# Kernel tuning notes

Measured on AMD Instinct MI355X. Metric: run time of the kernel, lower is better.

Reference implementation:

```python
import jax, jax.numpy as jnp
import numpy as np

B, T, C, H, D = 2, 2048, 1024, 16, 64


def setup_inputs() -> dict:
    key = jax.random.key(0)
    k1, k2, k3, k4, k5 = jax.random.split(key, 5)
    x = jax.random.normal(k1, (B, T, C), dtype=jnp.float32)
    Wq = jax.random.normal(k2, (H, C, D), dtype=jnp.float32) * 0.02
    Wk = jax.random.normal(k3, (H, C, D), dtype=jnp.float32) * 0.02
    Wv = jax.random.normal(k4, (H, C, D), dtype=jnp.float32) * 0.02
    Wo = jax.random.normal(k5, (C, C), dtype=jnp.float32) * 0.02
    bo = jnp.zeros((C,), dtype=jnp.float32)
    return {"x": x, "Wq": Wq, "Wk": Wk, "Wv": Wv, "Wo": Wo, "bo": bo}


def reference(x, Wq, Wk, Wv, Wo, bo):
    # per-head projections (batched over heads instead of a python loop)
    q = jnp.einsum('btc,hcd->bhtd', x, Wq)
    k = jnp.einsum('btc,hcd->bhtd', x, Wk)
    v = jnp.einsum('btc,hcd->bhtd', x, Wv)
    scale = jnp.asarray(D, x.dtype) ** -0.5
    wei = jnp.einsum('bhtd,bhsd->bhts', q, k) * scale  # [B,H,T,T]
    causal = jnp.tril(jnp.ones((T, T), dtype=bool))
    wei = jnp.where(causal, wei, jnp.asarray(-jnp.inf, wei.dtype))
    attn = jax.nn.softmax(wei, axis=-1)
    out = jnp.einsum('bhts,bhsd->bhtd', attn, v)  # [B,H,T,D]
    # concat heads (head order h0..hH-1 along feature dim)
    out = out.transpose(0, 2, 1, 3).reshape(B, T, C)
    # output projection: nn.Linear -> y = x @ W^T + b  (dropout p=0 is identity)
    return out @ Wo.T + bo
```

## Files before the change

kernel.cpp:

```cpp
#include <hip/hip_runtime.h>
#include <hip/hip_bf16.h>
#include <cstdint>
#include <math.h>

#define B_DIM 2
#define T_SEQ 2048
#define C_DIM 1024
#define H_NUM 16
#define D_HEAD 64
#define M_ROWS (B_DIM * T_SEQ)
#define N_QKV (3 * H_NUM * D_HEAD)

using short8  = __attribute__((ext_vector_type(8))) short;
using short4v = __attribute__((ext_vector_type(4))) short;
using f32x4   = __attribute__((ext_vector_type(4))) float;

__device__ __forceinline__ short f2bf(float f) {
  union { __hip_bfloat16 h; short s; } u;
  u.h = __float2bfloat16(f);
  return u.s;
}

__device__ __forceinline__ unsigned pk2bf(float a, float b) {
  union { float f; unsigned u; } ua, ub;
  ua.f = a; ub.f = b;
  return __builtin_amdgcn_perm(ub.u, ua.u, 0x07060302u);
}

__device__ __forceinline__ void gld_lds16(short* lds, const short* g) {
  __builtin_amdgcn_global_load_lds(
      (const unsigned int __attribute__((address_space(1)))*)g,
      (unsigned int __attribute__((address_space(3)))*)lds, 16, 0, 0);
}

#define BAR_VM(N)                                                    \
  do {                                                               \
    asm volatile("s_waitcnt vmcnt(" #N ") lgkmcnt(0)" ::: "memory"); \
    __builtin_amdgcn_s_barrier();                                    \
    __builtin_amdgcn_sched_barrier(0);                               \
  } while (0)

__global__ __launch_bounds__(256) void cvt_f32_bf16(const float* __restrict__ in,
                                                    short* __restrict__ out, int n8) {
  int i = blockIdx.x * 256 + threadIdx.x;
  if (i >= n8) return;
  const float4* p = reinterpret_cast<const float4*>(in) + (size_t)i * 2;
  float4 a = p[0], b = p[1];
  short8 o;
  o[0] = f2bf(a.x); o[1] = f2bf(a.y); o[2] = f2bf(a.z); o[3] = f2bf(a.w);
  o[4] = f2bf(b.x); o[5] = f2bf(b.y); o[6] = f2bf(b.z); o[7] = f2bf(b.w);
  reinterpret_cast<short8*>(out)[i] = o;
}

__global__ __launch_bounds__(256) void pack_w(const float* __restrict__ Wq,
                                              const float* __restrict__ Wk,
                                              const float* __restrict__ Wv,
                                              short* __restrict__ Wt) {
  int bid  = blockIdx.x;
  int proj = bid >> 8;
  int h    = (bid >> 4) & 15;
  int cb   = bid & 15;
  const float* W = (proj == 0) ? Wq : ((proj == 1) ? Wk : Wv);
  const float* src = W + ((size_t)h * C_DIM + (size_t)cb * 64) * D_HEAD;

  __shared__ float tile[64][65];
  int tid = threadIdx.x;

#pragma unroll
  for (int j = 0; j < 4; j++) {
    int flat = tid + j * 256;
    int c    = flat >> 4;
    int d4   = flat & 15;
    float4 v = reinterpret_cast<const float4*>(src + (size_t)c * D_HEAD)[d4];
    tile[c][d4 * 4 + 0] = v.x;
    tile[c][d4 * 4 + 1] = v.y;
    tile[c][d4 * 4 + 2] = v.z;
    tile[c][d4 * 4 + 3] = v.w;
  }
  __syncthreads();

  int d     = tid >> 2;
  int cpart = (tid & 3) * 16;
  short* dst = Wt + ((size_t)(proj * H_NUM + h) * D_HEAD + d) * C_DIM + cb * 64 + cpart;
  short8 o0, o1;
#pragma unroll
  for (int j = 0; j < 8; j++) {
    o0[j] = f2bf(tile[cpart + j][d]);
    o1[j] = f2bf(tile[cpart + 8 + j][d]);
  }
  *reinterpret_cast<short8*>(dst)     = o0;
  *reinterpret_cast<short8*>(dst + 8) = o1;
}

template <int MODE, int BMT>
__global__ __launch_bounds__(256) void gemm_bt(
    const short* __restrict__ A, const short* __restrict__ Bt,
    const float* __restrict__ bias,
    short* __restrict__ qb, short* __restrict__ kb, short* __restrict__ vtb,
    float* __restrict__ outb,
    int M, int N, int K) {
  constexpr int BK = 32;
  constexpr int MR = BMT / 32;
  constexpr int NLA = BMT / 64;
  __shared__ short As[3][BMT * BK];
  __shared__ short Bs[3][128 * BK];

  int tid  = threadIdx.x;
  int lane = tid & 63;
  int wv   = tid >> 6;
  int q15  = lane & 15, g = lane >> 4;
  int ntn  = N >> 7;
  int bm   = blockIdx.x / ntn;
  int bn   = blockIdx.x % ntn;
  int row0 = bm * BMT, col0 = bn << 7;
  int wm   = (wv >> 1) * (BMT / 2);
  int wn   = (wv & 1) << 6;

  f32x4 acc[MR][4];
#pragma unroll
  for (int i = 0; i < MR; i++)
#pragma unroll
    for (int j = 0; j < 4; j++) acc[i][j] = (f32x4){0.f, 0.f, 0.f, 0.f};

  const short* ag = A  + (size_t)(row0 + (tid >> 2)) * K + (tid & 3) * 8;
  const short* bg = Bt + (size_t)(col0 + (tid >> 2)) * K + (tid & 3) * 8;
  const size_t gstep = (size_t)64 * K;

  auto stage = [&](int ks, int buf) {
    const short* a  = ag + (size_t)ks * BK;
    const short* bb = bg + (size_t)ks * BK;
    gld_lds16(&As[buf][0] + tid * 8, a);
    if constexpr (NLA == 2) gld_lds16(&As[buf][64 * BK] + tid * 8, a + gstep);
    gld_lds16(&Bs[buf][0] + tid * 8, bb);
    gld_lds16(&Bs[buf][64 * BK] + tid * 8, bb + gstep);
  };

  int nk = K / BK;
  stage(0, 0);
  stage(1, 1);
  if constexpr (NLA == 2) {
    asm volatile("s_waitcnt vmcnt(4)" ::: "memory");
  } else {
    asm volatile("s_waitcnt vmcnt(3)" ::: "memory");
  }
  __builtin_amdgcn_s_barrier();
  __builtin_amdgcn_sched_barrier(0);

  for (int k = 0; k < nk; ++k) {
    int buf = k % 3;
    if (k + 2 < nk) stage(k + 2, (k + 2) % 3);

    short8 af[MR], bf[4];
#pragma unroll
    for (int mi = 0; mi < MR; mi++)
      af[mi] = *reinterpret_cast<const short8*>(
          &As[buf][(wm + mi * 16 + q15) * BK + g * 8]);
#pragma unroll
    for (int ni = 0; ni < 4; ni++)
      bf[ni] = *reinterpret_cast<const short8*>(
          &Bs[buf][(wn + ni * 16 + q15) * BK + g * 8]);
    __builtin_amdgcn_s_setprio(1);
#pragma unroll
    for (int mi = 0; mi < MR; mi++)
#pragma unroll
      for (int ni = 0; ni < 4; ni++)
        acc[mi][ni] = __builtin_amdgcn_mfma_f32_16x16x32_bf16(af[mi], bf[ni],
                                                              acc[mi][ni], 0, 0, 0);
    __builtin_amdgcn_s_setprio(0);

    if (k + 1 < nk) {
      if (k + 2 < nk) {
        if constexpr (NLA == 2) { BAR_VM(4); } else { BAR_VM(3); }
      } else {
        BAR_VM(0);
      }
    }
  }

#pragma unroll
  for (int mi = 0; mi < MR; mi++) {
#pragma unroll
    for (int ni = 0; ni < 4; ni++) {
      int rb  = row0 + wm + mi * 16 + (g << 2);
      int col = col0 + wn + ni * 16 + q15;
      f32x4 v = acc[mi][ni];
      if (MODE == 0) {
        int proj = col >> 10;
        int hh   = (col >> 6) & (H_NUM - 1);
        int d    = col & (D_HEAD - 1);
        int b    = rb >> 11;
        int t    = rb & (T_SEQ - 1);
        if (proj < 2) {
          float scl = (proj == 0) ? 0.125f * 1.44269504f : 1.0f;
          short* dst = (proj == 0 ? qb : kb) +
                       ((size_t)(b * H_NUM + hh) * T_SEQ) * D_HEAD + d;
#pragma unroll
          for (int r = 0; r < 4; r++)
            dst[(size_t)(t + r) * D_HEAD] = f2bf(v[r] * scl);
        } else {
          short4v pk;
#pragma unroll
          for (int r = 0; r < 4; r++) pk[r] = f2bf(v[r]);
          short* dst = vtb + ((size_t)(b * H_NUM + hh) * D_HEAD + d) * T_SEQ + t;
          *reinterpret_cast<short4v*>(dst) = pk;
        }
      } else {
        float bb = bias[col];
#pragma unroll
        for (int r = 0; r < 4; r++)
          outb[(size_t)(rb + r) * N + col] = v[r] + bb;
      }
    }
  }
}

__global__ __launch_bounds__(256, 4) void attn_fwd(const short* __restrict__ qg,
                                                   const short* __restrict__ kg,
                                                   const short* __restrict__ vt,
                                                   short* __restrict__ ob) {
  int bid  = blockIdx.x;
  int q2   = bid >> 8;
  int r    = bid & 255;
  int bh   = (r & 7) * 4 + q2;
  int sb   = r >> 3;
  int strip = (q2 & 1) ? sb : 31 - sb;
  int b    = bh >> 4;
  int h    = bh & 15;
  int tid  = threadIdx.x, lane = tid & 63, wv = tid >> 6;
  int q15  = lane & 15, g = lane >> 4;
  int qr   = strip * 64 + wv * 16;

  __shared__ short arena[16384];

  const short* qp = qg + (size_t)bh * T_SEQ * D_HEAD;
  const short* kp = kg + (size_t)bh * T_SEQ * D_HEAD;
  const short* vp = vt + (size_t)bh * D_HEAD * T_SEQ;

  int r8    = lane >> 3;
  int gcb   = ((lane & 7) * 16) ^ (r8 << 4);
  int srow0 = wv * 16;

  int hh = (q15 & 7) << 4;
  int koff0 = ((0 * 64 + g * 16) ^ hh) >> 1;
  int koff1 = ((1 * 64 + g * 16) ^ hh) >> 1;
  int voff[4];
#pragma unroll
  for (int st = 0; st < 4; st++) voff[st] = ((st * 32 + g * 8) ^ hh) >> 1;

  short8 qf[2];
#pragma unroll
  for (int kk = 0; kk < 2; kk++)
    qf[kk] = *reinterpret_cast<const short8*>(
        qp + (size_t)(qr + q15) * D_HEAD + kk * 32 + g * 8);

  f32x4 acc[4];
#pragma unroll
  for (int dt = 0; dt < 4; dt++) acc[dt] = (f32x4){0.f, 0.f, 0.f, 0.f};
  f32x4 lacc = (f32x4){0.f, 0.f, 0.f, 0.f};
  float m_ = -1e30f;

  const short4v ones4 = (short4v){(short)0x3F80, (short)0x3F80,
                                  (short)0x3F80, (short)0x3F80};

  int nch = strip + 1;

  auto stage = [&](int c, int pbuf) {
    const short* ks = kp + (size_t)(c * 64 + srow0 + r8) * D_HEAD + (gcb >> 1);
    const short* vs = vp + (size_t)(srow0 + r8) * T_SEQ + c * 64 + (gcb >> 1);
    short* kd = arena + pbuf * 4096 + srow0 * 64 + lane * 8;
    short* vd = arena + 8192 + pbuf * 4096 + srow0 * 64 + lane * 8;
    gld_lds16(kd, ks);
    gld_lds16(kd + 8 * 64, ks + (size_t)8 * D_HEAD);
    gld_lds16(vd, vs);
    gld_lds16(vd + 8 * 64, vs + (size_t)8 * T_SEQ);
  };

  stage(0, 0);
  BAR_VM(0);

  for (int c = 0; c < nch; ++c) {
    int s0 = c * 64;
    if (c + 1 < nch) stage(c + 1, (c + 1) & 1);
    const short* Kb = arena + (c & 1) * 4096;
    const short* Vb = arena + 8192 + (c & 1) * 4096;

    short8 kf[4][2];
#pragma unroll
    for (int st = 0; st < 4; st++) {
      int rbase = (st * 16 + q15) * 64;
      kf[st][0] = *reinterpret_cast<const short8*>(&Kb[rbase + koff0]);
      kf[st][1] = *reinterpret_cast<const short8*>(&Kb[rbase + koff1]);
    }

    f32x4 sv[4];
    __builtin_amdgcn_s_setprio(1);
#pragma unroll
    for (int st = 0; st < 4; st++) {
      f32x4 s = (f32x4){0.f, 0.f, 0.f, 0.f};
      s = __builtin_amdgcn_mfma_f32_16x16x32_bf16(kf[st][0], qf[0], s, 0, 0, 0);
      s = __builtin_amdgcn_mfma_f32_16x16x32_bf16(kf[st][1], qf[1], s, 0, 0, 0);
      sv[st] = s;
    }
    __builtin_amdgcn_s_setprio(0);

    short4v vf[4][4];
#pragma unroll
    for (int st = 0; st < 4; st++)
#pragma unroll
      for (int dt = 0; dt < 4; dt++)
        vf[st][dt] = *reinterpret_cast<const short4v*>(
            &Vb[(dt * 16 + q15) * 64 + voff[st]]);

    if (c == nch - 1) {
#pragma unroll
      for (int st = 0; st < 4; st++)
#pragma unroll
        for (int r2 = 0; r2 < 4; r2++) {
          int sg = s0 + st * 16 + g * 4 + r2;
          if (sg > qr + q15) sv[st][r2] = -1e30f;
        }
    }

    float t0 = fmaxf(fmaxf(sv[0][0], sv[0][1]), sv[0][2]);
    float t1 = fmaxf(fmaxf(sv[0][3], sv[1][0]), sv[1][1]);
    float t2 = fmaxf(fmaxf(sv[1][2], sv[1][3]), sv[2][0]);
    float t3 = fmaxf(fmaxf(sv[2][1], sv[2][2]), sv[2][3]);
    float t4 = fmaxf(fmaxf(sv[3][0], sv[3][1]), sv[3][2]);
    float mx = fmaxf(fmaxf(fmaxf(t0, t1), t2),
                     fmaxf(fmaxf(t3, t4), sv[3][3]));
    mx = fmaxf(mx, __shfl_xor(mx, 16));
    mx = fmaxf(mx, __shfl_xor(mx, 32));

    if (!__all(mx <= m_ + 11.5f)) {
      float mnew = fmaxf(m_, mx);
      float sc   = __builtin_amdgcn_exp2f(m_ - mnew);
      m_ = mnew;
      lacc *= sc;
#pragma unroll
      for (int dt = 0; dt < 4; dt++) acc[dt] *= sc;
    }
    float mcur = m_;

    short4v pbf[4];
#pragma unroll
    for (int st = 0; st < 4; st++) {
      float p0 = __builtin_amdgcn_exp2f(sv[st][0] - mcur);
      float p1 = __builtin_amdgcn_exp2f(sv[st][1] - mcur);
      float p2 = __builtin_amdgcn_exp2f(sv[st][2] - mcur);
      float p3 = __builtin_amdgcn_exp2f(sv[st][3] - mcur);
      union { short4v s; unsigned u[2]; } P;
      P.u[0] = pk2bf(p0, p1);
      P.u[1] = pk2bf(p2, p3);
      pbf[st] = P.s;
    }

    __builtin_amdgcn_s_setprio(1);
#pragma unroll
    for (int st = 0; st < 4; st++) {
#if __has_builtin(__builtin_amdgcn_mfma_f32_16x16x16bf16_1k)
      lacc = __builtin_amdgcn_mfma_f32_16x16x16bf16_1k(ones4, pbf[st], lacc, 0, 0, 0);
#pragma unroll
      for (int dt = 0; dt < 4; dt++)
        acc[dt] = __builtin_amdgcn_mfma_f32_16x16x16bf16_1k(
            vf[st][dt], pbf[st], acc[dt], 0, 0, 0);
#else
      short4v p4 = pbf[st];
      short8 bz = (short8){p4[0], p4[1], p4[2], p4[3], 0, 0, 0, 0};
      short8 oz = (short8){(short)0x3F80, (short)0x3F80, (short)0x3F80,
                           (short)0x3F80, 0, 0, 0, 0};
      lacc = __builtin_amdgcn_mfma_f32_16x16x32_bf16(oz, bz, lacc, 0, 0, 0);
#pragma unroll
      for (int dt = 0; dt < 4; dt++) {
        short4v v4 = vf[st][dt];
        short8 az = (short8){v4[0], v4[1], v4[2], v4[3], 0, 0, 0, 0};
        acc[dt] =
            __builtin_amdgcn_mfma_f32_16x16x32_bf16(az, bz, acc[dt], 0, 0, 0);
      }
#endif
    }
    __builtin_amdgcn_s_setprio(0);

    BAR_VM(0);
  }

  short* OlW = arena + wv * (16 * 68);
  float inv = 1.0f / lacc[0];
#pragma unroll
  for (int dt = 0; dt < 4; dt++)
#pragma unroll
    for (int r2 = 0; r2 < 4; r2++)
      OlW[q15 * 68 + dt * 16 + g * 4 + r2] = f2bf(acc[dt][r2] * inv);
  int row = lane >> 2, cb = (lane & 3) * 16;
  size_t base = ((size_t)(b * T_SEQ) + qr + row) * C_DIM + h * 64 + cb;
  const short* src = OlW + row * 68 + cb;
  *reinterpret_cast<short8*>(ob + base) = *reinterpret_cast<const short8*>(src);
  *reinterpret_cast<short8*>(ob + base + 8) =
      *reinterpret_cast<const short8*>(src + 8);
}

extern "C" void kernel_launch(void* const* d_in, const int* in_sizes, int n_in,
                              void* d_out, int out_size, void* d_ws, size_t ws_size,
                              hipStream_t stream) {
  const float* x  = (const float*)d_in[0];
  const float* Wq = (const float*)d_in[1];
  const float* Wk = (const float*)d_in[2];
  const float* Wv = (const float*)d_in[3];
  const float* Wo = (const float*)d_in[4];
  const float* bo = (const float*)d_in[5];
  float* out = (float*)d_out;

  char* ws = (char*)d_ws;
  short* xb   = (short*)(ws + 0);
  short* Wt   = (short*)(ws + 8388608);
  short* Wob  = (short*)(ws + 14680064);
  short* qb   = (short*)(ws + 16777216);
  short* kb   = (short*)(ws + 25165824);
  short* vtb  = (short*)(ws + 33554432);
  short* obuf = xb;

  cvt_f32_bf16<<<2048, 256, 0, stream>>>(x, xb, M_ROWS * C_DIM / 8);
  cvt_f32_bf16<<<512, 256, 0, stream>>>(Wo, Wob, C_DIM * C_DIM / 8);
  pack_w<<<768, 256, 0, stream>>>(Wq, Wk, Wv, Wt);

  gemm_bt<0, 128><<<(M_ROWS / 128) * (N_QKV / 128), 256, 0, stream>>>(
      xb, Wt, nullptr, qb, kb, vtb, nullptr, M_ROWS, N_QKV, C_DIM);

  attn_fwd<<<1024, 256, 0, stream>>>(qb, kb, vtb, obuf);

  gemm_bt<1, 64><<<(M_ROWS / 64) * (C_DIM / 128), 256, 0, stream>>>(
      obuf, Wob, bo, nullptr, nullptr, nullptr, out, M_ROWS, C_DIM, C_DIM);
}
```

Before: 115.2 us.

## Stage QKV GEMM epilogue through LDS for coalesced stores and XCD-aware tile mapping

The QKV projection epilogue now writes the bf16 accumulator tile into shared memory, then issues 16-byte coalesced row stores to the q/k and transposed v buffers. Previously it used scattered 2-byte and 8-byte stores. Block indices are also remapped so each XCD handles a contiguous range of M-tiles, aiming to improve L2 reuse of A rows. The change adds extra barriers and an LDS round-trip, and it assumes BMT=128 (LDT=136 and 8 passes of 16 rows) for the MODE 0 instantiation.

```diff
diff --git a/kernel.cpp b/kernel.cpp
--- a/kernel.cpp
+++ b/kernel.cpp
@@ -102,16 +102,20 @@
   constexpr int BK = 32;
   constexpr int MR = BMT / 32;
   constexpr int NLA = BMT / 64;
-  __shared__ short As[3][BMT * BK];
-  __shared__ short Bs[3][128 * BK];
+  __shared__ short GL[3 * (BMT + 128) * BK];
+  short* Asb = GL;
+  short* Bsb = GL + 3 * BMT * BK;
 
   int tid  = threadIdx.x;
   int lane = tid & 63;
   int wv   = tid >> 6;
   int q15  = lane & 15, g = lane >> 4;
   int ntn  = N >> 7;
-  int bm   = blockIdx.x / ntn;
-  int bn   = blockIdx.x % ntn;
+  int bpx  = (M / BMT) >> 3;
+  int xcd  = blockIdx.x & 7;
+  int idx  = blockIdx.x >> 3;
+  int bn   = idx / bpx;
+  int bm   = xcd * bpx + (idx - bn * bpx);
   int row0 = bm * BMT, col0 = bn << 7;
   int wm   = (wv >> 1) * (BMT / 2);
   int wn   = (wv & 1) << 6;
@@ -129,10 +133,11 @@
   auto stage = [&](int ks, int buf) {
     const short* a  = ag + (size_t)ks * BK;
     const short* bb = bg + (size_t)ks * BK;
-    gld_lds16(&As[buf][0] + tid * 8, a);
-    if constexpr (NLA == 2) gld_lds16(&As[buf][64 * BK] + tid * 8, a + gstep);
-    gld_lds16(&Bs[buf][0] + tid * 8, bb);
-    gld_lds16(&Bs[buf][64 * BK] + tid * 8, bb + gstep);
+    gld_lds16(Asb + buf * BMT * BK + tid * 8, a);
+    if constexpr (NLA == 2)
+      gld_lds16(Asb + buf * BMT * BK + 64 * BK + tid * 8, a + gstep);
+    gld_lds16(Bsb + buf * 128 * BK + tid * 8, bb);
+    gld_lds16(Bsb + buf * 128 * BK + 64 * BK + tid * 8, bb + gstep);
   };
 
   int nk = K / BK;
@@ -154,11 +159,11 @@
 #pragma unroll
     for (int mi = 0; mi < MR; mi++)
       af[mi] = *reinterpret_cast<const short8*>(
-          &As[buf][(wm + mi * 16 + q15) * BK + g * 8]);
+          &Asb[buf * BMT * BK + (wm + mi * 16 + q15) * BK + g * 8]);
 #pragma unroll
     for (int ni = 0; ni < 4; ni++)
       bf[ni] = *reinterpret_cast<const short8*>(
-          &Bs[buf][(wn + ni * 16 + q15) * BK + g * 8]);
+          &Bsb[buf * 128 * BK + (wn + ni * 16 + q15) * BK + g * 8]);
     __builtin_amdgcn_s_setprio(1);
 #pragma unroll
     for (int mi = 0; mi < MR; mi++)
@@ -177,34 +182,70 @@
     }
   }
 
-#pragma unroll
-  for (int mi = 0; mi < MR; mi++) {
-#pragma unroll
-    for (int ni = 0; ni < 4; ni++) {
-      int rb  = row0 + wm + mi * 16 + (g << 2);
-      int col = col0 + wn + ni * 16 + q15;
-      f32x4 v = acc[mi][ni];
-      if (MODE == 0) {
-        int proj = col >> 10;
-        int hh   = (col >> 6) & (H_NUM - 1);
-        int d    = col & (D_HEAD - 1);
-        int b    = rb >> 11;
-        int t    = rb & (T_SEQ - 1);
-        if (proj < 2) {
-          float scl = (proj == 0) ? 0.125f * 1.44269504f : 1.0f;
-          short* dst = (proj == 0 ? qb : kb) +
-                       ((size_t)(b * H_NUM + hh) * T_SEQ) * D_HEAD + d;
+  if constexpr (MODE == 0) {
+    constexpr int LDT = 136;
+    int proj  = col0 >> 10;
+    int b     = row0 >> 11;
+    int trow0 = row0 & (T_SEQ - 1);
+    int h0    = (col0 >> 6) & 15;
+    __syncthreads();
+    if (proj < 2) {
+      float scl = (proj == 0) ? 0.125f * 1.44269504f : 1.0f;
+#pragma unroll
+      for (int mi = 0; mi < MR; mi++)
+#pragma unroll
+        for (int ni = 0; ni < 4; ni++) {
+          int t0 = wm + mi * 16 + (g << 2);
+          int d2 = wn + ni * 16 + q15;
 #pragma unroll
           for (int r = 0; r < 4; r++)
-            dst[(size_t)(t + r) * D_HEAD] = f2bf(v[r] * scl);
-        } else {
+            GL[(t0 + r) * LDT + d2] = f2bf(acc[mi][ni][r] * scl);
+        }
+      __syncthreads();
+      short* dstb = (proj == 0) ? qb : kb;
+#pragma unroll
+      for (int ps = 0; ps < 8; ps++) {
+        int trow  = ps * 16 + (tid >> 4);
+        int chunk = tid & 15;
+        int hh    = h0 + (chunk >> 3);
+        int d     = (chunk & 7) * 8;
+        short8 v = *reinterpret_cast<const short8*>(&GL[trow * LDT + chunk * 8]);
+        *reinterpret_cast<short8*>(
+            dstb + ((size_t)(b * H_NUM + hh) * T_SEQ + trow0 + trow) * D_HEAD + d) = v;
+      }
+    } else {
+#pragma unroll
+      for (int mi = 0; mi < MR; mi++)
+#pragma unroll
+        for (int ni = 0; ni < 4; ni++) {
+          int t0 = wm + mi * 16 + (g << 2);
+          int d2 = wn + ni * 16 + q15;
           short4v pk;
 #pragma unroll
-          for (int r = 0; r < 4; r++) pk[r] = f2bf(v[r]);
-          short* dst = vtb + ((size_t)(b * H_NUM + hh) * D_HEAD + d) * T_SEQ + t;
-          *reinterpret_cast<short4v*>(dst) = pk;
+          for (int r = 0; r < 4; r++) pk[r] = f2bf(acc[mi][ni][r]);
+          *reinterpret_cast<short4v*>(&GL[d2 * LDT + t0]) = pk;
         }
-      } else {
+      __syncthreads();
+#pragma unroll
+      for (int ps = 0; ps < 8; ps++) {
+        int drow  = ps * 16 + (tid >> 4);
+        int chunk = tid & 15;
+        int hh    = h0 + (drow >> 6);
+        int d     = drow & 63;
+        short8 v = *reinterpret_cast<const short8*>(&GL[drow * LDT + chunk * 8]);
+        *reinterpret_cast<short8*>(
+            vtb + ((size_t)(b * H_NUM + hh) * D_HEAD + d) * T_SEQ + trow0 +
+            chunk * 8) = v;
+      }
+    }
+  } else {
+#pragma unroll
+    for (int mi = 0; mi < MR; mi++) {
+#pragma unroll
+      for (int ni = 0; ni < 4; ni++) {
+        int rb  = row0 + wm + mi * 16 + (g << 2);
+        int col = col0 + wn + ni * 16 + q15;
+        f32x4 v = acc[mi][ni];
         float bb = bias[col];
 #pragma unroll
         for (int r = 0; r < 4; r++)
```

Result: faster. 110.1 us (-4.4%).
